# Kernel tuning notes

Measured on AMD Instinct MI355X. Metric: run time of the kernel, lower is better.

The kernel has to match this reference:

```python
import jax, jax.numpy as jnp
import numpy as np

N_NODES = 50000
N_EDGES = 800000
N_GRAPHS = 64
IN_CH = 128
HID_CH = 128
FC_CH = 128


def setup_inputs() -> dict:
    key = jax.random.key(0)
    ks = jax.random.split(key, 12)

    def lin_w(k, fan_in, fan_out):
        return jax.random.normal(k, (fan_in, fan_out), jnp.float32) * (1.0 / np.sqrt(fan_in))

    return {
        "x": jax.random.normal(ks[0], (N_NODES, IN_CH), jnp.float32),
        "edge_index": jax.random.randint(ks[1], (2, N_EDGES), 0, N_NODES, dtype=jnp.int64),
        "batch_vec": jnp.sort(jax.random.randint(ks[2], (N_NODES,), 0, N_GRAPHS, dtype=jnp.int64)),
        "W1": lin_w(ks[3], IN_CH, HID_CH),
        "b1": jnp.zeros((HID_CH,), jnp.float32),
        "W2": lin_w(ks[4], HID_CH, HID_CH),
        "b2": jnp.zeros((HID_CH,), jnp.float32),
        "W3": lin_w(ks[5], HID_CH, FC_CH),
        "b3": jnp.zeros((FC_CH,), jnp.float32),
        "fcW1": lin_w(ks[6], FC_CH, IN_CH),
        "fcb1": jnp.zeros((IN_CH,), jnp.float32),
        "fcW2": lin_w(ks[7], IN_CH, 2),
        "fcb2": jnp.zeros((2,), jnp.float32),
    }


def reference(x, edge_index, batch_vec, W1, b1, W2, b2, W3, b3, fcW1, fcb1, fcW2, fcb2):
    n = x.shape[0]
    row, col = edge_index[0], edge_index[1]  # src -> dst

    # GCN symmetric normalization with self-loops: deg[j] = in-degree(j) + 1
    deg = jnp.zeros((n,), x.dtype).at[col].add(1.0) + 1.0
    inv_sqrt = jax.lax.rsqrt(deg)
    edge_norm = inv_sqrt[row] * inv_sqrt[col]  # [E]
    self_norm = (inv_sqrt * inv_sqrt)[:, None]  # [N,1], self-loop weight 1/deg

    def gcn(h, W, b):
        h = h @ W  # [N, out]
        agg = jnp.zeros_like(h).at[col].add(h[row] * edge_norm[:, None])
        return agg + h * self_norm + b

    h = jax.nn.relu(gcn(x, W1, b1))
    h = jax.nn.relu(gcn(h, W2, b2))
    h = jax.nn.relu(gcn(h, W3, b3))
    h = jax.nn.relu(h @ fcW1 + fcb1)
    h = h @ fcW2 + fcb2  # [N, 2]

    # global mean pool per graph
    sums = jax.ops.segment_sum(h, batch_vec, num_segments=N_GRAPHS)
    cnts = jax.ops.segment_sum(jnp.ones((n,), h.dtype), batch_vec, num_segments=N_GRAPHS)
    pooled = sums / jnp.maximum(cnts, 1.0)[:, None]  # [G, 2]
    return jax.nn.softmax(pooled, axis=1)
```

## Files before the change

### kernel.cpp

```cpp
#include <hip/hip_runtime.h>


#define CH 128
#define BSH 7
#define SEG 4096
#define EPW 4096
#define SA 40
#define SAF 136
#define SC 132
#define SC8 144

typedef unsigned short ushortT;
typedef unsigned int uintT;
typedef unsigned char ucharT;
typedef __attribute__((ext_vector_type(8))) short short8;
typedef __attribute__((ext_vector_type(4))) float floatx4;
typedef __attribute__((ext_vector_type(2))) float floatx2;

__device__ __forceinline__ float bf2f(uintT u) {
    return __uint_as_float(u << 16);
}
__device__ __forceinline__ ushortT f2bf(float f) {
    uintT x = __float_as_uint(f);
    return (ushortT)((x + 0x7fffu + ((x >> 16) & 1u)) >> 16);
}
__device__ __forceinline__ void dec4(uintT u, float* o) {
    floatx2 lo = __builtin_amdgcn_cvt_pk_f32_fp8((int)u, false);
    floatx2 hi = __builtin_amdgcn_cvt_pk_f32_fp8((int)u, true);
    o[0] = lo.x; o[1] = lo.y; o[2] = hi.x; o[3] = hi.y;
}
__device__ __forceinline__ void dec16(uint4 v, float* o) {
    dec4(v.x, o); dec4(v.y, o + 4); dec4(v.z, o + 8); dec4(v.w, o + 12);
}

__global__ __launch_bounds__(256) void k_bin(const int* __restrict__ row,
                                             const int* __restrict__ col,
                                             int* __restrict__ bfill,
                                             uintT* __restrict__ seg,
                                             int E, int NB) {
    __shared__ uintT staged[EPW];
    __shared__ int target[EPW];
    __shared__ int sval[512];
    __shared__ int horig[512];
    __shared__ int pcnt[512];
    __shared__ int gbase[512];
    const int t = threadIdx.x;
    const int e0 = blockIdx.x * EPW;
    const int cnt = min(EPW, E - e0);

    sval[t] = 0; sval[t + 256] = 0;
    __syncthreads();

    int er[16], ec[16];
#pragma unroll
    for (int i = 0; i < 16; ++i) {
        int le = i * 256 + t;
        if (le < cnt) {
            er[i] = row[e0 + le];
            ec[i] = col[e0 + le];
            atomicAdd(&sval[ec[i] >> BSH], 1);
        }
    }
    __syncthreads();
    horig[t] = sval[t]; horig[t + 256] = sval[t + 256];
    __syncthreads();
    for (int off = 1; off < 512; off <<= 1) {
        int a = (t >= off) ? sval[t - off] : 0;
        int b2 = sval[t + 256 - off];
        __syncthreads();
        sval[t] += a;
        sval[t + 256] += b2;
        __syncthreads();
    }
    for (int b = t; b < 512; b += 256) {
        int h = horig[b];
        pcnt[b] = sval[b] - h;
        gbase[b] = (h > 0 && b < NB) ? atomicAdd(&bfill[b], h) : 0;
    }
    __syncthreads();
#pragma unroll
    for (int i = 0; i < 16; ++i) {
        int le = i * 256 + t;
        if (le < cnt) {
            int b = ec[i] >> BSH;
            int j = atomicAdd(&pcnt[b], 1);
            staged[j] = (uintT)er[i] | ((uintT)ec[i] << 16);
            int lo = sval[b] - horig[b];
            target[j] = b * SEG + gbase[b] + (j - lo);
        }
    }
    __syncthreads();
    for (int s = t; s < cnt; s += 256) seg[target[s]] = staged[s];
}

__global__ __launch_bounds__(512) void k_binvs_bscan(const int* __restrict__ bfill,
                                                     const uintT* __restrict__ seg,
                                                     float* __restrict__ invs,
                                                     int* __restrict__ bbase,
                                                     int* __restrict__ indptr,
                                                     float* __restrict__ sums,
                                                     float* __restrict__ cnts,
                                                     int NB, int N, int E, int G) {
    const int b = blockIdx.x;
    const int t = threadIdx.x;
    if (b < NB) {
        __shared__ int h[128];
        if (t < 128) h[t] = 0;
        __syncthreads();
        int cnt = bfill[b];
        const uintT* sp = seg + (size_t)b * SEG;
        for (int s = t; s < cnt; s += 512) atomicAdd(&h[(sp[s] >> 16) & 127], 1);
        __syncthreads();
        int d = b * 128 + t;
        if (t < 128 && d < N) invs[d] = rsqrtf((float)h[t] + 1.0f);
    } else {
        __shared__ int s[512];
        for (int i = t; i < 3 * G; i += 512) {
            if (i < 2 * G) sums[i] = 0.f;
            else cnts[i - 2 * G] = 0.f;
        }
        int v = (t < NB) ? bfill[t] : 0;
        s[t] = v;
        __syncthreads();
        for (int off = 1; off < 512; off <<= 1) {
            int a = (t >= off) ? s[t - off] : 0;
            __syncthreads();
            s[t] += a;
            __syncthreads();
        }
        if (t < NB) bbase[t] = s[t] - v;
        if (t == 0) indptr[N] = E;
    }
}

__global__ __launch_bounds__(256) void k_scatterprep(const int* __restrict__ bfill,
                                                     const int* __restrict__ bbase,
                                                     const uintT* __restrict__ seg,
                                                     const float* __restrict__ invs,
                                                     int* __restrict__ indptr,
                                                     uintT* __restrict__ epack,
                                                     const float* __restrict__ X,
                                                     ucharT* __restrict__ Xb,
                                                     const float* __restrict__ w0,
                                                     const float* __restrict__ w1,
                                                     const float* __restrict__ w2,
                                                     const float* __restrict__ w3,
                                                     ushortT* __restrict__ Whi,
                                                     int N, int NB, int total4) {
    const int t = threadIdx.x;
    if ((int)blockIdx.x < NB) {
        __shared__ uintT staged[SEG];
        __shared__ int h[128];
        __shared__ int sc[128];
        __shared__ int pc[128];
        const int b = blockIdx.x;
        const int cnt = bfill[b];
        const int base = bbase[b];
        const uintT* sp = seg + (size_t)b * SEG;

        if (t < 128) h[t] = 0;
        __syncthreads();
        for (int s = t; s < cnt; s += 256) atomicAdd(&h[(sp[s] >> 16) & 127], 1);
        __syncthreads();
        if (t < 128) sc[t] = h[t];
        __syncthreads();
        for (int off = 1; off < 128; off <<= 1) {
            int a = (t >= off && t < 128) ? sc[t - off] : 0;
            __syncthreads();
            if (t < 128) sc[t] += a;
            __syncthreads();
        }
        if (t < 128) {
            int excl = sc[t] - h[t];
            pc[t] = excl;
            int d = b * 128 + t;
            if (d < N) indptr[d] = base + excl;
        }
        __syncthreads();
        for (int s = t; s < cnt; s += 256) {
            uintT rc = sp[s];
            int src = (int)(rc & 0xffffu), dst = (int)(rc >> 16);
            int j = atomicAdd(&pc[dst & 127], 1);
            float nrm = invs[src] * invs[dst];
            staged[j] = (uintT)src | ((uintT)f2bf(nrm) << 16);
        }
        __syncthreads();
        for (int s = t; s < cnt; s += 256) epack[base + s] = staged[s];
    } else if ((int)blockIdx.x < NB + 256) {
        int idx = (blockIdx.x - NB) * 256 + t;
        int m = idx >> 14;
        int r = idx & 16383;
        int n = r >> 7;
        int k = r & 127;
        const float* W = (m == 0) ? w0 : (m == 1) ? w1 : (m == 2) ? w2 : w3;
        Whi[m * 16384 + n * CH + k] = f2bf(W[k * CH + n]);
    } else {
        int i = (blockIdx.x - NB - 256) * 256 + t;
        if (i < total4) {
            float4 v = reinterpret_cast<const float4*>(X)[i];
            int r0 = __builtin_amdgcn_cvt_pk_fp8_f32(v.x, v.y, 0, false);
            int r1 = __builtin_amdgcn_cvt_pk_fp8_f32(v.z, v.w, r0, true);
            reinterpret_cast<int*>(Xb)[i] = r1;
        }
    }
}

__global__ __launch_bounds__(256) void k_agg(const ucharT* __restrict__ H8,
                                             const uintT* __restrict__ epack,
                                             const int* __restrict__ indptr,
                                             const float* __restrict__ invs,
                                             ucharT* __restrict__ Z8, int N) {
    const int wave = threadIdx.x >> 6, lane = threadIdx.x & 63;
    const int ng = lane >> 3;
    const int l = lane & 7;
    const int node = blockIdx.x * 32 + wave * 8 + ng;
    if (node >= N) return;

    const uint4* H4 = reinterpret_cast<const uint4*>(H8);

    float acc[16];
    {
        float sn = invs[node];
        float sn2 = sn * sn;
        float d[16];
        dec16(H4[(size_t)node * 8 + l], d);
#pragma unroll
        for (int j = 0; j < 16; ++j) acc[j] = sn2 * d[j];
    }

    int p = indptr[node];
    int p1 = indptr[node + 1];

    if (p + 8 <= p1) {
        uintT e0[8];
#pragma unroll
        for (int i = 0; i < 8; ++i) e0[i] = epack[p + i];
        for (; p + 16 <= p1; p += 8) {
            uintT e1[8];
#pragma unroll
            for (int i = 0; i < 8; ++i) e1[i] = epack[p + 8 + i];
            uint4 g[8];
#pragma unroll
            for (int i = 0; i < 8; ++i) g[i] = H4[(size_t)(int)(e0[i] & 0xffffu) * 8 + l];
#pragma unroll
            for (int i = 0; i < 8; ++i) {
                float wv = bf2f(e0[i] >> 16);
                float d[16];
                dec16(g[i], d);
#pragma unroll
                for (int j = 0; j < 16; ++j) acc[j] += wv * d[j];
            }
#pragma unroll
            for (int i = 0; i < 8; ++i) e0[i] = e1[i];
        }
        {
            uint4 g[8];
#pragma unroll
            for (int i = 0; i < 8; ++i) g[i] = H4[(size_t)(int)(e0[i] & 0xffffu) * 8 + l];
#pragma unroll
            for (int i = 0; i < 8; ++i) {
                float wv = bf2f(e0[i] >> 16);
                float d[16];
                dec16(g[i], d);
#pragma unroll
                for (int j = 0; j < 16; ++j) acc[j] += wv * d[j];
            }
            p += 8;
        }
    }
    int rem = p1 - p;
    if (rem > 0) {
        uintT e[8];
#pragma unroll
        for (int i = 0; i < 8; ++i) e[i] = epack[(i < rem) ? p + i : p];
        uint4 g[8];
#pragma unroll
        for (int i = 0; i < 8; ++i) g[i] = H4[(size_t)(int)(e[i] & 0xffffu) * 8 + l];
#pragma unroll
        for (int i = 0; i < 8; ++i) {
            float wv = (i < rem) ? bf2f(e[i] >> 16) : 0.f;
            float d[16];
            dec16(g[i], d);
#pragma unroll
            for (int j = 0; j < 16; ++j) acc[j] += wv * d[j];
        }
    }

    uint4 o;
    {
        int r0 = __builtin_amdgcn_cvt_pk_fp8_f32(acc[0], acc[1], 0, false);
        r0 = __builtin_amdgcn_cvt_pk_fp8_f32(acc[2], acc[3], r0, true);
        int r1 = __builtin_amdgcn_cvt_pk_fp8_f32(acc[4], acc[5], 0, false);
        r1 = __builtin_amdgcn_cvt_pk_fp8_f32(acc[6], acc[7], r1, true);
        int r2 = __builtin_amdgcn_cvt_pk_fp8_f32(acc[8], acc[9], 0, false);
        r2 = __builtin_amdgcn_cvt_pk_fp8_f32(acc[10], acc[11], r2, true);
        int r3 = __builtin_amdgcn_cvt_pk_fp8_f32(acc[12], acc[13], 0, false);
        r3 = __builtin_amdgcn_cvt_pk_fp8_f32(acc[14], acc[15], r3, true);
        o.x = (uintT)r0; o.y = (uintT)r1; o.z = (uintT)r2; o.w = (uintT)r3;
    }
    reinterpret_cast<uint4*>(Z8)[(size_t)node * 8 + l] = o;
}

__global__ __launch_bounds__(256) void k_gemm(const ucharT* __restrict__ In8,
                                              const ushortT* __restrict__ Whi,
                                              const float* __restrict__ Bias,
                                              ucharT* __restrict__ Out8, int N) {
    __shared__ ushortT smem[128 * SC];
    ushortT* As = smem;
    ushortT* Ws = smem + 128 * SA;
    ushortT* Cs = smem;

    const int tid = threadIdx.x;
    const int wave = tid >> 6, lane = tid & 63;
    const int quad = lane >> 4, l15 = lane & 15;
    const int mBase = (wave >> 1) * 64, nBase = (wave & 1) * 64;
    const int row0 = blockIdx.x * 128;
    const int r = tid >> 1, half = tid & 1;

    floatx4 acc[4][4];
    const floatx4 zero4 = {0.f, 0.f, 0.f, 0.f};
#pragma unroll
    for (int i = 0; i < 4; i++)
#pragma unroll
        for (int j = 0; j < 4; j++) acc[i][j] = zero4;

    for (int ks = 0; ks < 4; ++ks) {
        {
            int grow = row0 + r;
            uint4 a8 = {0, 0, 0, 0};
            if (grow < N)
                a8 = *reinterpret_cast<const uint4*>(
                    In8 + (size_t)grow * CH + ks * 32 + half * 16);
            uintT wds[4] = {a8.x, a8.y, a8.z, a8.w};
            uintT ob[8];
#pragma unroll
            for (int q = 0; q < 4; ++q) {
                float d[4];
                dec4(wds[q], d);
                ob[2 * q] = (uintT)f2bf(d[0]) | ((uintT)f2bf(d[1]) << 16);
                ob[2 * q + 1] = (uintT)f2bf(d[2]) | ((uintT)f2bf(d[3]) << 16);
            }
            uint4* dd = reinterpret_cast<uint4*>(&As[r * SA + half * 16]);
            dd[0] = uint4{ob[0], ob[1], ob[2], ob[3]};
            dd[1] = uint4{ob[4], ob[5], ob[6], ob[7]};
            const uint4* sh = reinterpret_cast<const uint4*>(Whi + r * CH + ks * 32 + half * 16);
            uint4* dh = reinterpret_cast<uint4*>(&Ws[r * SA + half * 16]);
            dh[0] = sh[0]; dh[1] = sh[1];
        }
        __syncthreads();

        short8 af[4], wf[4];
#pragma unroll
        for (int mt = 0; mt < 4; ++mt)
            af[mt] = *reinterpret_cast<const short8*>(&As[(mBase + mt * 16 + l15) * SA + quad * 8]);
#pragma unroll
        for (int nt = 0; nt < 4; ++nt)
            wf[nt] = *reinterpret_cast<const short8*>(&Ws[(nBase + nt * 16 + l15) * SA + quad * 8]);
#pragma unroll
        for (int mt = 0; mt < 4; ++mt)
#pragma unroll
            for (int nt = 0; nt < 4; ++nt)
                acc[mt][nt] = __builtin_amdgcn_mfma_f32_16x16x32_bf16(af[mt], wf[nt], acc[mt][nt], 0, 0, 0);
        __syncthreads();
    }

    float bb[4];
#pragma unroll
    for (int nt = 0; nt < 4; ++nt) bb[nt] = Bias[nBase + nt * 16 + l15];

    ucharT* Cs8 = reinterpret_cast<ucharT*>(Cs);
#pragma unroll
    for (int mt = 0; mt < 4; ++mt)
#pragma unroll
        for (int nt = 0; nt < 4; ++nt)
#pragma unroll
            for (int r4 = 0; r4 < 4; ++r4) {
                int lrow = mBase + mt * 16 + quad * 4 + r4;
                float v = fmaxf(acc[mt][nt][r4] + bb[nt], 0.f);
                int f8 = __builtin_amdgcn_cvt_pk_fp8_f32(v, 0.f, 0, false);
                Cs8[lrow * SC8 + nBase + nt * 16 + l15] = (ucharT)(f8 & 0xff);
            }
    __syncthreads();
    {
        int grow = row0 + r;
        if (grow < N) {
            const uint4* s4 = reinterpret_cast<const uint4*>(&Cs8[r * SC8 + half * 64]);
            uint4* dst = reinterpret_cast<uint4*>(Out8 + (size_t)grow * CH + half * 64);
#pragma unroll
            for (int q = 0; q < 4; ++q) dst[q] = s4[q];
        }
    }
}

__global__ __launch_bounds__(256) void k_tail(const ucharT* __restrict__ Z8,
                                              const ushortT* __restrict__ W3hi,
                                              const float* __restrict__ B3,
                                              const ushortT* __restrict__ F1hi,
                                              const float* __restrict__ FB1,
                                              const float* __restrict__ FW2,
                                              const float* __restrict__ FB2,
                                              const int* __restrict__ batch,
                                              float* __restrict__ sums,
                                              float* __restrict__ cnts, int N) {
    __shared__ ushortT Hf[128 * SAF];
    __shared__ ushortT Ws[128 * SA];
    __shared__ float rp0[256];
    __shared__ float rp1[256];
    __shared__ float ls[192];

    const int tid = threadIdx.x;
    const int wave = tid >> 6, lane = tid & 63;
    const int quad = lane >> 4, l15 = lane & 15;
    const int mBase = (wave >> 1) * 64, nBase = (wave & 1) * 64;
    const int row0 = blockIdx.x * 128;
    const int r = tid >> 1, half = tid & 1;

    {
        int grow = row0 + r;
        uint4 a8 = {0, 0, 0, 0}, b8 = {0, 0, 0, 0}, c8 = {0, 0, 0, 0}, d8v = {0, 0, 0, 0};
        if (grow < N) {
            const uint4* s = reinterpret_cast<const uint4*>(Z8 + (size_t)grow * CH + half * 64);
            a8 = s[0]; b8 = s[1]; c8 = s[2]; d8v = s[3];
        }
        uintT wds[16] = {a8.x, a8.y, a8.z, a8.w, b8.x, b8.y, b8.z, b8.w,
                         c8.x, c8.y, c8.z, c8.w, d8v.x, d8v.y, d8v.z, d8v.w};
#pragma unroll
        for (int q = 0; q < 16; ++q) {
            float d[4];
            dec4(wds[q], d);
            uint2 o;
            o.x = (uintT)f2bf(d[0]) | ((uintT)f2bf(d[1]) << 16);
            o.y = (uintT)f2bf(d[2]) | ((uintT)f2bf(d[3]) << 16);
            *reinterpret_cast<uint2*>(&Hf[r * SAF + half * 64 + q * 4]) = o;
        }
    }

    floatx4 acc[4][4];
    const floatx4 zero4 = {0.f, 0.f, 0.f, 0.f};
#pragma unroll
    for (int i = 0; i < 4; i++)
#pragma unroll
        for (int j = 0; j < 4; j++) acc[i][j] = zero4;

    for (int ks = 0; ks < 4; ++ks) {
        {
            const uint4* sh = reinterpret_cast<const uint4*>(W3hi + r * CH + ks * 32 + half * 16);
            uint4* dh = reinterpret_cast<uint4*>(&Ws[r * SA + half * 16]);
            dh[0] = sh[0]; dh[1] = sh[1];
        }
        __syncthreads();
        short8 af[4], wf[4];
#pragma unroll
        for (int mt = 0; mt < 4; ++mt)
            af[mt] = *reinterpret_cast<const short8*>(&Hf[(mBase + mt * 16 + l15) * SAF + ks * 32 + quad * 8]);
#pragma unroll
        for (int nt = 0; nt < 4; ++nt)
            wf[nt] = *reinterpret_cast<const short8*>(&Ws[(nBase + nt * 16 + l15) * SA + quad * 8]);
#pragma unroll
        for (int mt = 0; mt < 4; ++mt)
#pragma unroll
            for (int nt = 0; nt < 4; ++nt)
                acc[mt][nt] = __builtin_amdgcn_mfma_f32_16x16x32_bf16(af[mt], wf[nt], acc[mt][nt], 0, 0, 0);
        __syncthreads();
    }

    {
        float bb[4];
#pragma unroll
        for (int nt = 0; nt < 4; ++nt) bb[nt] = B3[nBase + nt * 16 + l15];
#pragma unroll
        for (int mt = 0; mt < 4; ++mt)
#pragma unroll
            for (int nt = 0; nt < 4; ++nt)
#pragma unroll
                for (int r4 = 0; r4 < 4; ++r4) {
                    int lrow = mBase + mt * 16 + quad * 4 + r4;
                    float v = fmaxf(acc[mt][nt][r4] + bb[nt], 0.f);
                    Hf[lrow * SAF + nBase + nt * 16 + l15] = f2bf(v);
                }
    }
    __syncthreads();

#pragma unroll
    for (int i = 0; i < 4; i++)
#pragma unroll
        for (int j = 0; j < 4; j++) acc[i][j] = zero4;
    for (int ks = 0; ks < 4; ++ks) {
        {
            const uint4* sh = reinterpret_cast<const uint4*>(F1hi + r * CH + ks * 32 + half * 16);
            uint4* dh = reinterpret_cast<uint4*>(&Ws[r * SA + half * 16]);
            dh[0] = sh[0]; dh[1] = sh[1];
        }
        __syncthreads();
        short8 af[4], wf[4];
#pragma unroll
        for (int mt = 0; mt < 4; ++mt)
            af[mt] = *reinterpret_cast<const short8*>(&Hf[(mBase + mt * 16 + l15) * SAF + ks * 32 + quad * 8]);
#pragma unroll
        for (int nt = 0; nt < 4; ++nt)
            wf[nt] = *reinterpret_cast<const short8*>(&Ws[(nBase + nt * 16 + l15) * SA + quad * 8]);
#pragma unroll
        for (int mt = 0; mt < 4; ++mt)
#pragma unroll
            for (int nt = 0; nt < 4; ++nt)
                acc[mt][nt] = __builtin_amdgcn_mfma_f32_16x16x32_bf16(af[mt], wf[nt], acc[mt][nt], 0, 0, 0);
        __syncthreads();
    }

    {
        float bb[4];
#pragma unroll
        for (int nt = 0; nt < 4; ++nt) bb[nt] = FB1[nBase + nt * 16 + l15];
        float w20[4], w21[4];
#pragma unroll
        for (int nt = 0; nt < 4; ++nt) {
            float2 wv = *reinterpret_cast<const float2*>(FW2 + 2 * (nBase + nt * 16 + l15));
            w20[nt] = wv.x;
            w21[nt] = wv.y;
        }
#pragma unroll
        for (int mt = 0; mt < 4; ++mt)
#pragma unroll
            for (int r4 = 0; r4 < 4; ++r4) {
                float d0 = 0.f, d1 = 0.f;
#pragma unroll
                for (int nt = 0; nt < 4; ++nt) {
                    float v = fmaxf(acc[mt][nt][r4] + bb[nt], 0.f);
                    d0 += v * w20[nt];
                    d1 += v * w21[nt];
                }
#pragma unroll
                for (int m = 8; m >= 1; m >>= 1) {
                    d0 += __shfl_xor(d0, m, 64);
                    d1 += __shfl_xor(d1, m, 64);
                }
                if (l15 == 0) {
                    int lrow = mBase + mt * 16 + quad * 4 + r4;
                    rp0[lrow * 2 + (wave & 1)] = d0;
                    rp1[lrow * 2 + (wave & 1)] = d1;
                }
            }
    }
    if (tid < 192) ls[tid] = 0.f;
    __syncthreads();

    if (tid < 128) {
        int node = row0 + tid;
        if (node < N) {
            float d0 = rp0[tid * 2] + rp0[tid * 2 + 1] + FB2[0];
            float d1 = rp1[tid * 2] + rp1[tid * 2 + 1] + FB2[1];
            int g = batch[node];
            atomicAdd(&ls[g], d0);
            atomicAdd(&ls[64 + g], d1);
            atomicAdd(&ls[128 + g], 1.0f);
        }
    }
    __syncthreads();
    if (tid < 64) {
        float c = ls[128 + tid];
        if (c != 0.f) {
            atomicAdd(&sums[2 * tid], ls[tid]);
            atomicAdd(&sums[2 * tid + 1], ls[64 + tid]);
            atomicAdd(&cnts[tid], c);
        }
    }
}

__global__ void k_softmax(const float* __restrict__ sums, const float* __restrict__ cnts,
                          float* __restrict__ out, int G) {
    int g = blockIdx.x * blockDim.x + threadIdx.x;
    if (g < G) {
        float c = fmaxf(cnts[g], 1.0f);
        float p0 = sums[2 * g] / c;
        float p1 = sums[2 * g + 1] / c;
        float m = fmaxf(p0, p1);
        float e0 = expf(p0 - m), e1 = expf(p1 - m);
        float inv = 1.f / (e0 + e1);
        out[2 * g] = e0 * inv;
        out[2 * g + 1] = e1 * inv;
    }
}

extern "C" void kernel_launch(void* const* d_in, const int* in_sizes, int n_in,
                              void* d_out, int out_size, void* d_ws, size_t ws_size,
                              hipStream_t stream) {
    const float* X   = (const float*)d_in[0];
    const int* EI    = (const int*)d_in[1];
    const int* BATCH = (const int*)d_in[2];
    const float* W1  = (const float*)d_in[3];
    const float* B1  = (const float*)d_in[4];
    const float* W2  = (const float*)d_in[5];
    const float* B2  = (const float*)d_in[6];
    const float* W3  = (const float*)d_in[7];
    const float* B3  = (const float*)d_in[8];
    const float* FW1 = (const float*)d_in[9];
    const float* FB1 = (const float*)d_in[10];
    const float* FW2 = (const float*)d_in[11];
    const float* FB2 = (const float*)d_in[12];

    const int N = in_sizes[0] / CH;
    const int E = in_sizes[1] / 2;
    const int G = out_size / 2;
    const int* rowp = EI;
    const int* colp = EI + E;
    const int NB = (N + 127) >> BSH;

    char* w = (char*)d_ws;
    auto alloc = [&](size_t bytes) -> char* {
        char* p = w;
        w += (bytes + 255) & ~(size_t)255;
        return p;
    };
    ucharT*  Z8    = (ucharT*)alloc((size_t)N * CH);
    ucharT*  Hb8   = (ucharT*)alloc((size_t)N * CH);
    ucharT*  Xb8   = (ucharT*)alloc((size_t)N * CH);
    ushortT* WhiA  = (ushortT*)alloc((size_t)4 * 16384 * 2);
    float* invs    = (float*)alloc((size_t)N * 4);
    int*   indptr  = (int*)alloc((size_t)(N + 1) * 4);
    uintT* epack   = (uintT*)alloc((size_t)E * 4);
    uintT* seg     = (uintT*)alloc((size_t)NB * SEG * 4);
    int*   bfill   = (int*)alloc((size_t)NB * 4);
    int*   bbase   = (int*)alloc((size_t)NB * 4);
    float* sums    = (float*)alloc((size_t)G * 3 * 4);
    float* cnts    = sums + 2 * G;

    const int nbAgg  = (N + 31) / 32;
    const int nbGemm = (N + 127) / 128;
    const int nbBin  = (E + EPW - 1) / EPW;
    const int total4 = N * CH / 4;
    const int nbSP   = NB + 256 + (total4 + 255) / 256;

    hipMemsetAsync(bfill, 0, (size_t)NB * 4, stream);
    k_bin<<<nbBin, 256, 0, stream>>>(rowp, colp, bfill, seg, E, NB);
    k_binvs_bscan<<<NB + 1, 512, 0, stream>>>(bfill, seg, invs, bbase, indptr,
                                              sums, cnts, NB, N, E, G);
    k_scatterprep<<<nbSP, 256, 0, stream>>>(bfill, bbase, seg, invs, indptr, epack,
                                            X, Xb8, W1, W2, W3, FW1, WhiA, N, NB, total4);

    k_agg<<<nbAgg, 256, 0, stream>>>(Xb8, epack, indptr, invs, Z8, N);
    k_gemm<<<nbGemm, 256, 0, stream>>>(Z8, WhiA, B1, Hb8, N);
    k_agg<<<nbAgg, 256, 0, stream>>>(Hb8, epack, indptr, invs, Z8, N);
    k_gemm<<<nbGemm, 256, 0, stream>>>(Z8, WhiA + 16384, B2, Hb8, N);
    k_agg<<<nbAgg, 256, 0, stream>>>(Hb8, epack, indptr, invs, Z8, N);
    k_tail<<<nbGemm, 256, 0, stream>>>(Z8, WhiA + 2 * 16384, B3,
                                       WhiA + 3 * 16384, FB1, FW2, FB2,
                                       BATCH, sums, cnts, N);
    k_softmax<<<1, 64, 0, stream>>>(sums, cnts, (float*)d_out, G);
}
```

Before: 209.4 us.

## Fuse softmax into tail, move conversions into bin kernel, stage full K tiles

Moves the weight transpose/bf16 conversion and the fp8 conversion of X out of the scatter kernel and into extra blocks of the binning kernel, so they run alongside edge binning. The GEMM and tail kernels now load the whole 128-wide K slice of activations and weights into LDS once, replacing four K-step loads each with a barrier. The separate softmax launch is dropped: the last block to finish the tail kernel, detected with a global atomic counter, computes the pooled softmax. This removes launches and barriers but uses more LDS per block, which may lower occupancy, and relies on the atomic last-block pattern.

```diff
diff --git a/kernel.cpp b/kernel.cpp
--- a/kernel.cpp
+++ b/kernel.cpp
@@ -5,9 +5,7 @@
 #define BSH 7
 #define SEG 4096
 #define EPW 4096
-#define SA 40
 #define SAF 136
-#define SC 132
 #define SC8 144
 
 typedef unsigned short ushortT;
@@ -37,7 +35,14 @@
                                              const int* __restrict__ col,
                                              int* __restrict__ bfill,
                                              uintT* __restrict__ seg,
-                                             int E, int NB) {
+                                             const float* __restrict__ X,
+                                             ucharT* __restrict__ Xb,
+                                             const float* __restrict__ w0,
+                                             const float* __restrict__ w1,
+                                             const float* __restrict__ w2,
+                                             const float* __restrict__ w3,
+                                             ushortT* __restrict__ Whi,
+                                             int E, int NBB, int NB, int total4) {
     __shared__ uintT staged[EPW];
     __shared__ int target[EPW];
     __shared__ int sval[512];
@@ -45,6 +50,28 @@
     __shared__ int pcnt[512];
     __shared__ int gbase[512];
     const int t = threadIdx.x;
+
+    if ((int)blockIdx.x >= NBB) {
+        if ((int)blockIdx.x < NBB + 256) {
+            int idx = ((int)blockIdx.x - NBB) * 256 + t;
+            int m = idx >> 14;
+            int r2 = idx & 16383;
+            int n = r2 >> 7;
+            int k = r2 & 127;
+            const float* W = (m == 0) ? w0 : (m == 1) ? w1 : (m == 2) ? w2 : w3;
+            Whi[m * 16384 + n * CH + k] = f2bf(W[k * CH + n]);
+        } else {
+            int i = ((int)blockIdx.x - NBB - 256) * 256 + t;
+            if (i < total4) {
+                float4 v = reinterpret_cast<const float4*>(X)[i];
+                int r0 = __builtin_amdgcn_cvt_pk_fp8_f32(v.x, v.y, 0, false);
+                int r1 = __builtin_amdgcn_cvt_pk_fp8_f32(v.z, v.w, r0, true);
+                reinterpret_cast<int*>(Xb)[i] = r1;
+            }
+        }
+        return;
+    }
+
     const int e0 = blockIdx.x * EPW;
     const int cnt = min(EPW, E - e0);
 
@@ -100,6 +127,7 @@
                                                      int* __restrict__ indptr,
                                                      float* __restrict__ sums,
                                                      float* __restrict__ cnts,
+                                                     int* __restrict__ tdone,
                                                      int NB, int N, int E, int G) {
     const int b = blockIdx.x;
     const int t = threadIdx.x;
@@ -119,6 +147,7 @@
             if (i < 2 * G) sums[i] = 0.f;
             else cnts[i - 2 * G] = 0.f;
         }
+        if (t == 0) atomicExch(tdone, 0);
         int v = (t < NB) ? bfill[t] : 0;
         s[t] = v;
         __syncthreads();
@@ -133,76 +162,51 @@
     }
 }
 
-__global__ __launch_bounds__(256) void k_scatterprep(const int* __restrict__ bfill,
-                                                     const int* __restrict__ bbase,
-                                                     const uintT* __restrict__ seg,
-                                                     const float* __restrict__ invs,
-                                                     int* __restrict__ indptr,
-                                                     uintT* __restrict__ epack,
-                                                     const float* __restrict__ X,
-                                                     ucharT* __restrict__ Xb,
-                                                     const float* __restrict__ w0,
-                                                     const float* __restrict__ w1,
-                                                     const float* __restrict__ w2,
-                                                     const float* __restrict__ w3,
-                                                     ushortT* __restrict__ Whi,
-                                                     int N, int NB, int total4) {
+__global__ __launch_bounds__(256) void k_scatter(const int* __restrict__ bfill,
+                                                 const int* __restrict__ bbase,
+                                                 const uintT* __restrict__ seg,
+                                                 const float* __restrict__ invs,
+                                                 int* __restrict__ indptr,
+                                                 uintT* __restrict__ epack,
+                                                 int N) {
+    __shared__ uintT staged[SEG];
+    __shared__ int h[128];
+    __shared__ int sc[128];
+    __shared__ int pc[128];
     const int t = threadIdx.x;
-    if ((int)blockIdx.x < NB) {
-        __shared__ uintT staged[SEG];
-        __shared__ int h[128];
-        __shared__ int sc[128];
-        __shared__ int pc[128];
-        const int b = blockIdx.x;
-        const int cnt = bfill[b];
-        const int base = bbase[b];
-        const uintT* sp = seg + (size_t)b * SEG;
-
-        if (t < 128) h[t] = 0;
+    const int b = blockIdx.x;
+    const int cnt = bfill[b];
+    const int base = bbase[b];
+    const uintT* sp = seg + (size_t)b * SEG;
+
+    if (t < 128) h[t] = 0;
+    __syncthreads();
+    for (int s = t; s < cnt; s += 256) atomicAdd(&h[(sp[s] >> 16) & 127], 1);
+    __syncthreads();
+    if (t < 128) sc[t] = h[t];
+    __syncthreads();
+    for (int off = 1; off < 128; off <<= 1) {
+        int a = (t >= off && t < 128) ? sc[t - off] : 0;
         __syncthreads();
-        for (int s = t; s < cnt; s += 256) atomicAdd(&h[(sp[s] >> 16) & 127], 1);
+        if (t < 128) sc[t] += a;
         __syncthreads();
-        if (t < 128) sc[t] = h[t];
-        __syncthreads();
-        for (int off = 1; off < 128; off <<= 1) {
-            int a = (t >= off && t < 128) ? sc[t - off] : 0;
-            __syncthreads();
-            if (t < 128) sc[t] += a;
-            __syncthreads();
-        }
-        if (t < 128) {
-            int excl = sc[t] - h[t];
-            pc[t] = excl;
-            int d = b * 128 + t;
-            if (d < N) indptr[d] = base + excl;
-        }
-        __syncthreads();
-        for (int s = t; s < cnt; s += 256) {
-            uintT rc = sp[s];
-            int src = (int)(rc & 0xffffu), dst = (int)(rc >> 16);
-            int j = atomicAdd(&pc[dst & 127], 1);
-            float nrm = invs[src] * invs[dst];
-            staged[j] = (uintT)src | ((uintT)f2bf(nrm) << 16);
-        }
-        __syncthreads();
-        for (int s = t; s < cnt; s += 256) epack[base + s] = staged[s];
-    } else if ((int)blockIdx.x < NB + 256) {
-        int idx = (blockIdx.x - NB) * 256 + t;
-        int m = idx >> 14;
-        int r = idx & 16383;
-        int n = r >> 7;
-        int k = r & 127;
-        const float* W = (m == 0) ? w0 : (m == 1) ? w1 : (m == 2) ? w2 : w3;
-        Whi[m * 16384 + n * CH + k] = f2bf(W[k * CH + n]);
-    } else {
-        int i = (blockIdx.x - NB - 256) * 256 + t;
-        if (i < total4) {
-            float4 v = reinterpret_cast<const float4*>(X)[i];
-            int r0 = __builtin_amdgcn_cvt_pk_fp8_f32(v.x, v.y, 0, false);
-            int r1 = __builtin_amdgcn_cvt_pk_fp8_f32(v.z, v.w, r0, true);
-            reinterpret_cast<int*>(Xb)[i] = r1;
-        }
-    }
+    }
+    if (t < 128) {
+        int excl = sc[t] - h[t];
+        pc[t] = excl;
+        int d = b * 128 + t;
+        if (d < N) indptr[d] = base + excl;
+    }
+    __syncthreads();
+    for (int s = t; s < cnt; s += 256) {
+        uintT rc = sp[s];
+        int src = (int)(rc & 0xffffu), dst = (int)(rc >> 16);
+        int j = atomicAdd(&pc[dst & 127], 1);
+        float nrm = invs[src] * invs[dst];
+        staged[j] = (uintT)src | ((uintT)f2bf(nrm) << 16);
+    }
+    __syncthreads();
+    for (int s = t; s < cnt; s += 256) epack[base + s] = staged[s];
 }
 
 __global__ __launch_bounds__(256) void k_agg(const ucharT* __restrict__ H8,
@@ -305,10 +309,8 @@
                                               const ushortT* __restrict__ Whi,
                                               const float* __restrict__ Bias,
                                               ucharT* __restrict__ Out8, int N) {
-    __shared__ ushortT smem[128 * SC];
-    ushortT* As = smem;
-    ushortT* Ws = smem + 128 * SA;
-    ushortT* Cs = smem;
+    __shared__ ushortT As[128 * SAF];
+    __shared__ ushortT Ws[128 * SAF];
 
     const int tid = threadIdx.x;
     const int wave = tid >> 6, lane = tid & 63;
@@ -317,6 +319,31 @@
     const int row0 = blockIdx.x * 128;
     const int r = tid >> 1, half = tid & 1;
 
+    {
+        int grow = row0 + r;
+        uint4 a8 = {0, 0, 0, 0}, b8 = {0, 0, 0, 0}, c8 = {0, 0, 0, 0}, d8v = {0, 0, 0, 0};
+        if (grow < N) {
+            const uint4* s = reinterpret_cast<const uint4*>(In8 + (size_t)grow * CH + half * 64);
+            a8 = s[0]; b8 = s[1]; c8 = s[2]; d8v = s[3];
+        }
+        uintT wds[16] = {a8.x, a8.y, a8.z, a8.w, b8.x, b8.y, b8.z, b8.w,
+                         c8.x, c8.y, c8.z, c8.w, d8v.x, d8v.y, d8v.z, d8v.w};
+#pragma unroll
+        for (int q = 0; q < 16; ++q) {
+            float d[4];
+            dec4(wds[q], d);
+            uint2 o;
+            o.x = (uintT)f2bf(d[0]) | ((uintT)f2bf(d[1]) << 16);
+            o.y = (uintT)f2bf(d[2]) | ((uintT)f2bf(d[3]) << 16);
+            *reinterpret_cast<uint2*>(&As[r * SAF + half * 64 + q * 4]) = o;
+        }
+        const uint4* sh = reinterpret_cast<const uint4*>(Whi + r * CH + half * 64);
+#pragma unroll
+        for (int q = 0; q < 8; ++q)
+            *reinterpret_cast<uint4*>(&Ws[r * SAF + half * 64 + q * 8]) = sh[q];
+    }
+    __syncthreads();
+
     floatx4 acc[4][4];
     const floatx4 zero4 = {0.f, 0.f, 0.f, 0.f};
 #pragma unroll
@@ -324,51 +351,28 @@
 #pragma unroll
         for (int j = 0; j < 4; j++) acc[i][j] = zero4;
 
+#pragma unroll
     for (int ks = 0; ks < 4; ++ks) {
-        {
-            int grow = row0 + r;
-            uint4 a8 = {0, 0, 0, 0};
-            if (grow < N)
-                a8 = *reinterpret_cast<const uint4*>(
-                    In8 + (size_t)grow * CH + ks * 32 + half * 16);
-            uintT wds[4] = {a8.x, a8.y, a8.z, a8.w};
-            uintT ob[8];
-#pragma unroll
-            for (int q = 0; q < 4; ++q) {
-                float d[4];
-                dec4(wds[q], d);
-                ob[2 * q] = (uintT)f2bf(d[0]) | ((uintT)f2bf(d[1]) << 16);
-                ob[2 * q + 1] = (uintT)f2bf(d[2]) | ((uintT)f2bf(d[3]) << 16);
-            }
-            uint4* dd = reinterpret_cast<uint4*>(&As[r * SA + half * 16]);
-            dd[0] = uint4{ob[0], ob[1], ob[2], ob[3]};
-            dd[1] = uint4{ob[4], ob[5], ob[6], ob[7]};
-            const uint4* sh = reinterpret_cast<const uint4*>(Whi + r * CH + ks * 32 + half * 16);
-            uint4* dh = reinterpret_cast<uint4*>(&Ws[r * SA + half * 16]);
-            dh[0] = sh[0]; dh[1] = sh[1];
-        }
-        __syncthreads();
-
         short8 af[4], wf[4];
 #pragma unroll
         for (int mt = 0; mt < 4; ++mt)
-            af[mt] = *reinterpret_cast<const short8*>(&As[(mBase + mt * 16 + l15) * SA + quad * 8]);
+            af[mt] = *reinterpret_cast<const short8*>(&As[(mBase + mt * 16 + l15) * SAF + ks * 32 + quad * 8]);
 #pragma unroll
         for (int nt = 0; nt < 4; ++nt)
-            wf[nt] = *reinterpret_cast<const short8*>(&Ws[(nBase + nt * 16 + l15) * SA + quad * 8]);
+            wf[nt] = *reinterpret_cast<const short8*>(&Ws[(nBase + nt * 16 + l15) * SAF + ks * 32 + quad * 8]);
 #pragma unroll
         for (int mt = 0; mt < 4; ++mt)
 #pragma unroll
             for (int nt = 0; nt < 4; ++nt)
                 acc[mt][nt] = __builtin_amdgcn_mfma_f32_16x16x32_bf16(af[mt], wf[nt], acc[mt][nt], 0, 0, 0);
-        __syncthreads();
-    }
+    }
+    __syncthreads();
 
     float bb[4];
 #pragma unroll
     for (int nt = 0; nt < 4; ++nt) bb[nt] = Bias[nBase + nt * 16 + l15];
 
-    ucharT* Cs8 = reinterpret_cast<ucharT*>(Cs);
+    ucharT* Cs8 = reinterpret_cast<ucharT*>(As);
 #pragma unroll
     for (int mt = 0; mt < 4; ++mt)
 #pragma unroll
@@ -401,12 +405,16 @@
                                               const float* __restrict__ FB2,
                                               const int* __restrict__ batch,
                                               float* __restrict__ sums,
-                                              float* __restrict__ cnts, int N) {
+                                              float* __restrict__ cnts,
+                                              float* __restrict__ out,
+                                              int* __restrict__ tdone,
+                                              int N, int G) {
     __shared__ ushortT Hf[128 * SAF];
-    __shared__ ushortT Ws[128 * SA];
+    __shared__ ushortT Ws[128 * SAF];
     __shared__ float rp0[256];
     __shared__ float rp1[256];
     __shared__ float ls[192];
+    __shared__ int lastFlag;
 
     const int tid = threadIdx.x;
     const int wave = tid >> 6, lane = tid & 63;
@@ -433,7 +441,12 @@
             o.y = (uintT)f2bf(d[2]) | ((uintT)f2bf(d[3]) << 16);
             *reinterpret_cast<uint2*>(&Hf[r * SAF + half * 64 + q * 4]) = o;
         }
-    }
+        const uint4* sh = reinterpret_cast<const uint4*>(W3hi + r * CH + half * 64);
+#pragma unroll
+        for (int q = 0; q < 8; ++q)
+            *reinterpret_cast<uint4*>(&Ws[r * SAF + half * 64 + q * 8]) = sh[q];
+    }
+    __syncthreads();
 
     floatx4 acc[4][4];
     const floatx4 zero4 = {0.f, 0.f, 0.f, 0.f};
@@ -442,27 +455,22 @@
 #pragma unroll
         for (int j = 0; j < 4; j++) acc[i][j] = zero4;
 
+#pragma unroll
     for (int ks = 0; ks < 4; ++ks) {
-        {
-            const uint4* sh = reinterpret_cast<const uint4*>(W3hi + r * CH + ks * 32 + half * 16);
-            uint4* dh = reinterpret_cast<uint4*>(&Ws[r * SA + half * 16]);
-            dh[0] = sh[0]; dh[1] = sh[1];
-        }
-        __syncthreads();
         short8 af[4], wf[4];
 #pragma unroll
         for (int mt = 0; mt < 4; ++mt)
             af[mt] = *reinterpret_cast<const short8*>(&Hf[(mBase + mt * 16 + l15) * SAF + ks * 32 + quad * 8]);
 #pragma unroll
         for (int nt = 0; nt < 4; ++nt)
-            wf[nt] = *reinterpret_cast<const short8*>(&Ws[(nBase + nt * 16 + l15) * SA + quad * 8]);
+            wf[nt] = *reinterpret_cast<const short8*>(&Ws[(nBase + nt * 16 + l15) * SAF + ks * 32 + quad * 8]);
 #pragma unroll
         for (int mt = 0; mt < 4; ++mt)
 #pragma unroll
             for (int nt = 0; nt < 4; ++nt)
                 acc[mt][nt] = __builtin_amdgcn_mfma_f32_16x16x32_bf16(af[mt], wf[nt], acc[mt][nt], 0, 0, 0);
-        __syncthreads();
-    }
+    }
+    __syncthreads();
 
     {
         float bb[4];
@@ -478,6 +486,10 @@
                     float v = fmaxf(acc[mt][nt][r4] + bb[nt], 0.f);
                     Hf[lrow * SAF + nBase + nt * 16 + l15] = f2bf(v);
                 }
+        const uint4* sh = reinterpret_cast<const uint4*>(F1hi + r * CH + half * 64);
+#pragma unroll
+        for (int q = 0; q < 8; ++q)
+            *reinterpret_cast<uint4*>(&Ws[r * SAF + half * 64 + q * 8]) = sh[q];
     }
     __syncthreads();
 
@@ -485,26 +497,20 @@
     for (int i = 0; i < 4; i++)
 #pragma unroll
         for (int j = 0; j < 4; j++) acc[i][j] = zero4;
+#pragma unroll
     for (int ks = 0; ks < 4; ++ks) {
-        {
-            const uint4* sh = reinterpret_cast<const uint4*>(F1hi + r * CH + ks * 32 + half * 16);
-            uint4* dh = reinterpret_cast<uint4*>(&Ws[r * SA + half * 16]);
-            dh[0] = sh[0]; dh[1] = sh[1];
-        }
-        __syncthreads();
         short8 af[4], wf[4];
 #pragma unroll
         for (int mt = 0; mt < 4; ++mt)
             af[mt] = *reinterpret_cast<const short8*>(&Hf[(mBase + mt * 16 + l15) * SAF + ks * 32 + quad * 8]);
 #pragma unroll
         for (int nt = 0; nt < 4; ++nt)
-            wf[nt] = *reinterpret_cast<const short8*>(&Ws[(nBase + nt * 16 + l15) * SA + quad * 8]);
+            wf[nt] = *reinterpret_cast<const short8*>(&Ws[(nBase + nt * 16 + l15) * SAF + ks * 32 + quad * 8]);
 #pragma unroll
         for (int mt = 0; mt < 4; ++mt)
 #pragma unroll
             for (int nt = 0; nt < 4; ++nt)
                 acc[mt][nt] = __builtin_amdgcn_mfma_f32_16x16x32_bf16(af[mt], wf[nt], acc[mt][nt], 0, 0, 0);
-        __syncthreads();
     }
 
     {
@@ -564,15 +570,18 @@
             atomicAdd(&cnts[tid], c);
         }
     }
-}
-
-__global__ void k_softmax(const float* __restrict__ sums, const float* __restrict__ cnts,
-                          float* __restrict__ out, int G) {
-    int g = blockIdx.x * blockDim.x + threadIdx.x;
-    if (g < G) {
-        float c = fmaxf(cnts[g], 1.0f);
-        float p0 = sums[2 * g] / c;
-        float p1 = sums[2 * g + 1] / c;
+    __syncthreads();
+
+    if (tid == 0) {
+        int old = atomicAdd(tdone, 1);
+        lastFlag = (old == (int)gridDim.x - 1) ? 1 : 0;
+    }
+    __syncthreads();
+    if (lastFlag && tid < G) {
+        int g = tid;
+        float c = fmaxf(atomicAdd(&cnts[g], 0.f), 1.0f);
+        float p0 = atomicAdd(&sums[2 * g], 0.f) / c;
+        float p1 = atomicAdd(&sums[2 * g + 1], 0.f) / c;
         float m = fmaxf(p0, p1);
         float e0 = expf(p0 - m), e1 = expf(p1 - m);
         float inv = 1.f / (e0 + e1);
@@ -623,19 +632,21 @@
     int*   bbase   = (int*)alloc((size_t)NB * 4);
     float* sums    = (float*)alloc((size_t)G * 3 * 4);
     float* cnts    = sums + 2 * G;
+    int*   tdone   = (int*)alloc(256);
 
     const int nbAgg  = (N + 31) / 32;
     const int nbGemm = (N + 127) / 128;
     const int nbBin  = (E + EPW - 1) / EPW;
     const int total4 = N * CH / 4;
-    const int nbSP   = NB + 256 + (total4 + 255) / 256;
+    const int nbXc   = (total4 + 255) / 256;
 
     hipMemsetAsync(bfill, 0, (size_t)NB * 4, stream);
-    k_bin<<<nbBin, 256, 0, stream>>>(rowp, colp, bfill, seg, E, NB);
+    k_bin<<<nbBin + 256 + nbXc, 256, 0, stream>>>(rowp, colp, bfill, seg,
+                                                  X, Xb8, W1, W2, W3, FW1, WhiA,
+                                                  E, nbBin, NB, total4);
     k_binvs_bscan<<<NB + 1, 512, 0, stream>>>(bfill, seg, invs, bbase, indptr,
-                                              sums, cnts, NB, N, E, G);
-    k_scatterprep<<<nbSP, 256, 0, stream>>>(bfill, bbase, seg, invs, indptr, epack,
-                                            X, Xb8, W1, W2, W3, FW1, WhiA, N, NB, total4);
+                                              sums, cnts, tdone, NB, N, E, G);
+    k_scatter<<<NB, 256, 0, stream>>>(bfill, bbase, seg, invs, indptr, epack, N);
 
     k_agg<<<nbAgg, 256, 0, stream>>>(Xb8, epack, indptr, invs, Z8, N);
     k_gemm<<<nbGemm, 256, 0, stream>>>(Z8, WhiA, B1, Hb8, N);
@@ -644,6 +655,5 @@
     k_agg<<<nbAgg, 256, 0, stream>>>(Hb8, epack, indptr, invs, Z8, N);
     k_tail<<<nbGemm, 256, 0, stream>>>(Z8, WhiA + 2 * 16384, B3,
                                        WhiA + 3 * 16384, FB1, FW2, FB2,
-                                       BATCH, sums, cnts, N);
-    k_softmax<<<1, 64, 0, stream>>>(sums, cnts, (float*)d_out, G);
-}
+                                       BATCH, sums, cnts, (float*)d_out, tdone, N, G);
+}
```

After: 204.2 us. -2.5%, faster.
